# Performance work log

Measured on AMD Instinct MI355X. Metric: run time of the kernel, lower is better.

The kernel has to match this reference:

```python
import jax, jax.numpy as jnp
import numpy as np

M = 7
KSIZE = M + 1          # kernel height = 8
PAD = KSIZE // 2       # conv padding on seq dim = 4 -> output length L+1
NUM_KERNELS = 74


def setup_inputs() -> dict:
    key = jax.random.key(0)
    kx, kk = jax.random.split(key)
    x = jax.random.normal(kx, (256, 512, 7), dtype=jnp.float32)
    kernels = jax.random.normal(kk, (NUM_KERNELS, KSIZE, 3), dtype=jnp.float32)
    return {"x": x, "kernels": kernels}


def reference(x, kernels):
    # x: (B, L, C); kernels: (74, 8, 3)
    B, L, C = x.shape
    # Width-3 conv over width-1 input with padding 1: only the middle kernel
    # column (index 1) multiplies real data; the side columns hit zero padding.
    keff = kernels[:, :, 1]  # (74, 8)
    # Seq-dim cross-correlation with padding 4 and kernel 8 -> output length L+1.
    xp = jnp.pad(x, ((0, 0), (PAD, PAD), (0, 0)))  # (B, L+8, C)
    idx = jnp.arange(L + 1)[:, None] + jnp.arange(KSIZE)[None, :]  # (L+1, 8)
    win = xp[:, idx, :]  # (B, L+1, 8, C) sliding windows
    # First 73 kernels applied to every channel; outputs ordered channel-major
    # (channel outer, kernel inner) to match the torch append order.
    out_main = jnp.einsum('btjc,kj->btck', win, keff[:NUM_KERNELS - 1])
    out_main = out_main.reshape(B, L + 1, C * (NUM_KERNELS - 1))
    # Last kernel applied to one 'random' channel; fixed to channel 0 for
    # a deterministic reference (torch uses torch.randint at runtime).
    out_last = jnp.einsum('btj,j->bt', win[:, :, :, 0], keff[NUM_KERNELS - 1])
    out = jnp.concatenate([out_main, out_last[..., None]], axis=-1)  # (B, L+1, 73*C+1)
    # Faithful to torch: reshape (L+1)*(73*C+1) elems into (B, L, -1);
    # valid because 73*C+1 == 512 is divisible by L == 512.
    return out.reshape(B, L, -1)
```

## Files before the change

### kernel.cpp

```cpp
#include <hip/hip_runtime.h>


typedef float v2f __attribute__((ext_vector_type(2)));
typedef float v4f __attribute__((ext_vector_type(4)));

#define CDIM 7
#define TROWS 513
#define CHUNK 64
#define WIN_ROWS 72
#define WIN_ELEMS (WIN_ROWS * CDIM)

__device__ __forceinline__ int chan_of(int f) { return (f == 511) ? 0 : (f / 73); }
__device__ __forceinline__ int kidx_of(int f) { return (f == 511) ? 73 : (f % 73); }

__global__ __launch_bounds__(256, 8) void tok_conv_kernel(
    const float* __restrict__ x,
    const float* __restrict__ kern,
    float* __restrict__ out)
{
  __shared__ __align__(16) float lds[WIN_ELEMS];

  const int tid   = threadIdx.x;
  const int b     = blockIdx.y;
  const int chunk = blockIdx.x;
  const float* xb = x + b * (512 * CDIM);

  const int f0 = 2 * tid, f1 = f0 + 1;
  const int c0 = chan_of(f0), k0 = kidx_of(f0);
  const int c1 = chan_of(f1), k1 = kidx_of(f1);

  v2f kp[8];
#pragma unroll
  for (int j = 0; j < 8; ++j)
    kp[j] = (v2f){kern[k0 * 24 + j * 3 + 1], kern[k1 * 24 + j * 3 + 1]};

  if (chunk == 8) {
    v2f acc = {0.f, 0.f};
#pragma unroll
    for (int j = 0; j < 8; ++j) {
      const int p   = 508 + j;
      const bool ok = p < 512;
      const int bse = (ok ? p : 0) * CDIM;
      v2f w;
      w.x = ok ? xb[bse + c0] : 0.f;
      w.y = ok ? xb[bse + c1] : 0.f;
      acc += w * kp[j];
    }
    reinterpret_cast<v2f*>(out + ((size_t)b * TROWS + 512) * 512)[tid] = acc;
    return;
  }

  const int t0 = chunk * CHUNK;

  if (chunk >= 1 && chunk <= 6) {
    const v4f* src = reinterpret_cast<const v4f*>(xb + (t0 - 4) * CDIM);
    if (tid < WIN_ELEMS / 4)
      reinterpret_cast<v4f*>(lds)[tid] = src[tid];
  } else {
#pragma unroll
    for (int i = tid; i < WIN_ELEMS; i += 256) {
      const int r = i / CDIM;
      const int c = i - r * CDIM;
      const int p = t0 - 4 + r;
      lds[i] = ((unsigned)p < 512u) ? xb[p * CDIM + c] : 0.f;
    }
  }
  __syncthreads();

  int bx0 = c0, bx1 = c1;

  v2f w[8];
#pragma unroll
  for (int j = 0; j < 8; ++j)
    w[j] = (v2f){lds[bx0 + j * CDIM], lds[bx1 + j * CDIM]};

  v2f* orow = reinterpret_cast<v2f*>(out + ((size_t)b * TROWS + t0) * 512) + tid;

#pragma unroll 1
  for (int g = 0; g < 8; ++g) {
#pragma unroll
    for (int u = 0; u < 8; ++u) {
      v2f nv;
      nv.x = lds[bx0 + (u + 8) * CDIM];
      nv.y = lds[bx1 + (u + 8) * CDIM];

      v2f acc = {0.f, 0.f};
#pragma unroll
      for (int j = 0; j < 8; ++j)
        acc += w[(u + j) & 7] * kp[j];

      *orow = acc;
      orow += 256;

      w[u & 7] = nv;
    }
    bx0 += 8 * CDIM;
    bx1 += 8 * CDIM;
  }
}

extern "C" void kernel_launch(void* const* d_in, const int* in_sizes, int n_in,
                              void* d_out, int out_size, void* d_ws, size_t ws_size,
                              hipStream_t stream) {
  const float* x    = (const float*)d_in[0];
  const float* kern = (const float*)d_in[1];
  float* out        = (float*)d_out;

  dim3 grid(9, 256);
  tok_conv_kernel<<<grid, 256, 0, stream>>>(x, kern, out);
}
```

Baseline: 55.59 us.

## Use 16-byte output stores with paired-channel LDS layout and two-row interleave

Each thread now computes four adjacent output features per row and writes them as one 16-byte store, with the two halves of the block covering alternating rows. A second LDS staging pass rearranges the input window into channel pairs, so each sliding-window read is a single 8-byte load, including pairs that straddle two channels. The goal is fewer, wider global stores and fewer LDS reads per output. In exchange the kernel adds an extra LDS pass, an extra barrier and more registers, and the launch-bounds occupancy hint drops from 8 to 5.

```diff
diff --git a/kernel.cpp b/kernel.cpp
--- a/kernel.cpp
+++ b/kernel.cpp
@@ -8,33 +8,34 @@
 #define TROWS 513
 #define CHUNK 64
 #define WIN_ROWS 72
-#define WIN_ELEMS (WIN_ROWS * CDIM)
+#define RAW_ELEMS (WIN_ROWS * CDIM)
+#define NPAIRS 11
+#define PAIR_ITEMS (WIN_ROWS * NPAIRS)
 
 __device__ __forceinline__ int chan_of(int f) { return (f == 511) ? 0 : (f / 73); }
 __device__ __forceinline__ int kidx_of(int f) { return (f == 511) ? 73 : (f % 73); }
+__device__ __forceinline__ int pair_m(int f) {
+  const int cA = chan_of(f), cB = chan_of(f + 1);
+  return (cA == cB) ? cA : (cA == 6 ? 10 : 7 + (cA >> 1));
+}
 
-__global__ __launch_bounds__(256, 8) void tok_conv_kernel(
+__global__ __launch_bounds__(256, 5) void tok_conv_kernel(
     const float* __restrict__ x,
     const float* __restrict__ kern,
     float* __restrict__ out)
 {
-  __shared__ __align__(16) float lds[WIN_ELEMS];
+  __shared__ __align__(16) float raw[RAW_ELEMS];
+  __shared__ __align__(8)  v2f  pairs[PAIR_ITEMS];
 
   const int tid   = threadIdx.x;
   const int b     = blockIdx.y;
   const int chunk = blockIdx.x;
   const float* xb = x + b * (512 * CDIM);
 
-  const int f0 = 2 * tid, f1 = f0 + 1;
-  const int c0 = chan_of(f0), k0 = kidx_of(f0);
-  const int c1 = chan_of(f1), k1 = kidx_of(f1);
-
-  v2f kp[8];
-#pragma unroll
-  for (int j = 0; j < 8; ++j)
-    kp[j] = (v2f){kern[k0 * 24 + j * 3 + 1], kern[k1 * 24 + j * 3 + 1]};
-
   if (chunk == 8) {
+    const int f0 = 2 * tid, f1 = f0 + 1;
+    const int c0 = chan_of(f0), k0 = kidx_of(f0);
+    const int c1 = chan_of(f1), k1 = kidx_of(f1);
     v2f acc = {0.f, 0.f};
 #pragma unroll
     for (int j = 0; j < 8; ++j) {
@@ -44,58 +45,98 @@
       v2f w;
       w.x = ok ? xb[bse + c0] : 0.f;
       w.y = ok ? xb[bse + c1] : 0.f;
-      acc += w * kp[j];
+      const v2f kpj = {kern[k0 * 24 + j * 3 + 1], kern[k1 * 24 + j * 3 + 1]};
+      acc += w * kpj;
     }
     reinterpret_cast<v2f*>(out + ((size_t)b * TROWS + 512) * 512)[tid] = acc;
     return;
+  }
+
+  const int q    = tid & 127;
+  const int rpar = tid >> 7;
+  const int f0   = 4 * q;
+  const int m01  = pair_m(f0);
+  const int m23  = pair_m(f0 + 2);
+
+  v2f kp01[8], kp23[8];
+  {
+    const int k0 = kidx_of(f0),     k1 = kidx_of(f0 + 1);
+    const int k2 = kidx_of(f0 + 2), k3 = kidx_of(f0 + 3);
+#pragma unroll
+    for (int j = 0; j < 8; ++j) {
+      kp01[j] = (v2f){kern[k0 * 24 + j * 3 + 1], kern[k1 * 24 + j * 3 + 1]};
+      kp23[j] = (v2f){kern[k2 * 24 + j * 3 + 1], kern[k3 * 24 + j * 3 + 1]};
+    }
   }
 
   const int t0 = chunk * CHUNK;
 
   if (chunk >= 1 && chunk <= 6) {
     const v4f* src = reinterpret_cast<const v4f*>(xb + (t0 - 4) * CDIM);
-    if (tid < WIN_ELEMS / 4)
-      reinterpret_cast<v4f*>(lds)[tid] = src[tid];
+    if (tid < RAW_ELEMS / 4)
+      reinterpret_cast<v4f*>(raw)[tid] = src[tid];
   } else {
 #pragma unroll
-    for (int i = tid; i < WIN_ELEMS; i += 256) {
+    for (int i = tid; i < RAW_ELEMS; i += 256) {
       const int r = i / CDIM;
       const int c = i - r * CDIM;
       const int p = t0 - 4 + r;
-      lds[i] = ((unsigned)p < 512u) ? xb[p * CDIM + c] : 0.f;
+      raw[i] = ((unsigned)p < 512u) ? xb[p * CDIM + c] : 0.f;
     }
   }
   __syncthreads();
 
-  int bx0 = c0, bx1 = c1;
+#pragma unroll
+  for (int item = tid; item < PAIR_ITEMS; item += 256) {
+    const int r = item / NPAIRS;
+    const int m = item - r * NPAIRS;
+    const int cA = (m < 7) ? m : 2 * (m - 7);
+    const int cB = (m < 7) ? m : ((m == 10) ? 0 : cA + 1);
+    pairs[item] = (v2f){raw[r * CDIM + cA], raw[r * CDIM + cB]};
+  }
+  __syncthreads();
 
-  v2f w[8];
+  const v2f* pp01 = pairs + (rpar * NPAIRS + m01);
+  const v2f* pp23 = pairs + (rpar * NPAIRS + m23);
+
+  v2f wp01[8], wp23[8];
 #pragma unroll
-  for (int j = 0; j < 8; ++j)
-    w[j] = (v2f){lds[bx0 + j * CDIM], lds[bx1 + j * CDIM]};
+  for (int j = 0; j < 8; ++j) {
+    wp01[j] = pp01[j * NPAIRS];
+    wp23[j] = pp23[j * NPAIRS];
+  }
 
-  v2f* orow = reinterpret_cast<v2f*>(out + ((size_t)b * TROWS + t0) * 512) + tid;
+  v4f* orow =
+      reinterpret_cast<v4f*>(out + ((size_t)b * TROWS + t0 + rpar) * 512) + q;
 
 #pragma unroll 1
   for (int g = 0; g < 8; ++g) {
 #pragma unroll
-    for (int u = 0; u < 8; ++u) {
-      v2f nv;
-      nv.x = lds[bx0 + (u + 8) * CDIM];
-      nv.y = lds[bx1 + (u + 8) * CDIM];
+    for (int u = 0; u < 4; ++u) {
+      const int base = 2 * u;
 
-      v2f acc = {0.f, 0.f};
+      const v2f n01a = pp01[(base + 8) * NPAIRS];
+      const v2f n01b = pp01[(base + 9) * NPAIRS];
+      const v2f n23a = pp23[(base + 8) * NPAIRS];
+      const v2f n23b = pp23[(base + 9) * NPAIRS];
+
+      v2f a01 = {0.f, 0.f}, a23 = {0.f, 0.f};
 #pragma unroll
-      for (int j = 0; j < 8; ++j)
-        acc += w[(u + j) & 7] * kp[j];
+      for (int j = 0; j < 8; ++j) {
+        a01 += wp01[(base + j) & 7] * kp01[j];
+        a23 += wp23[(base + j) & 7] * kp23[j];
+      }
+      const v4f o = {a01.x, a01.y, a23.x, a23.y};
+      *orow = o;
+      orow += 2 * 128;
 
-      *orow = acc;
-      orow += 256;
-
-      w[u & 7] = nv;
+      wp01[base & 7]       = n01a;
+      wp01[(base + 1) & 7] = n01b;
+      wp23[base & 7]       = n23a;
+      wp23[(base + 1) & 7] = n23b;
     }
-    bx0 += 8 * CDIM;
-    bx1 += 8 * CDIM;
+    pp01 += 8 * NPAIRS;
+    pp23 += 8 * NPAIRS;
   }
 }
 
```

Measured after the change: 62.20 us. 11.9% more time.

## Stage output rows through double-buffered LDS for 16-byte global stores

Applied to the files above, without the earlier changes.

Each block now writes its computed outputs into two LDS buffers of four rows each instead of storing 8-byte values straight to global memory. It then copies each finished buffer to global memory with 16-byte vector stores, alternating buffers so the stores of one group overlap the computation of the next. The aim is wider, better-coalesced writes for this store-bound kernel. In exchange it adds 16 KB of LDS per block and two barriers per iteration, which may lower occupancy.

```diff
diff --git a/kernel.cpp b/kernel.cpp
--- a/kernel.cpp
+++ b/kernel.cpp
@@ -8,7 +8,7 @@
 #define TROWS 513
 #define CHUNK 64
 #define WIN_ROWS 72
-#define WIN_ELEMS (WIN_ROWS * CDIM)
+#define RAW_ELEMS (WIN_ROWS * CDIM)
 
 __device__ __forceinline__ int chan_of(int f) { return (f == 511) ? 0 : (f / 73); }
 __device__ __forceinline__ int kidx_of(int f) { return (f == 511) ? 73 : (f % 73); }
@@ -18,7 +18,9 @@
     const float* __restrict__ kern,
     float* __restrict__ out)
 {
-  __shared__ __align__(16) float lds[WIN_ELEMS];
+  __shared__ __align__(16) float raw[RAW_ELEMS];
+  __shared__ __align__(16) float buf0[4 * 512];
+  __shared__ __align__(16) float buf1[4 * 512];
 
   const int tid   = threadIdx.x;
   const int b     = blockIdx.y;
@@ -54,15 +56,15 @@
 
   if (chunk >= 1 && chunk <= 6) {
     const v4f* src = reinterpret_cast<const v4f*>(xb + (t0 - 4) * CDIM);
-    if (tid < WIN_ELEMS / 4)
-      reinterpret_cast<v4f*>(lds)[tid] = src[tid];
+    if (tid < RAW_ELEMS / 4)
+      reinterpret_cast<v4f*>(raw)[tid] = src[tid];
   } else {
 #pragma unroll
-    for (int i = tid; i < WIN_ELEMS; i += 256) {
+    for (int i = tid; i < RAW_ELEMS; i += 256) {
       const int r = i / CDIM;
       const int c = i - r * CDIM;
       const int p = t0 - 4 + r;
-      lds[i] = ((unsigned)p < 512u) ? xb[p * CDIM + c] : 0.f;
+      raw[i] = ((unsigned)p < 512u) ? xb[p * CDIM + c] : 0.f;
     }
   }
   __syncthreads();
@@ -72,31 +74,53 @@
   v2f w[8];
 #pragma unroll
   for (int j = 0; j < 8; ++j)
-    w[j] = (v2f){lds[bx0 + j * CDIM], lds[bx1 + j * CDIM]};
+    w[j] = (v2f){raw[bx0 + j * CDIM], raw[bx1 + j * CDIM]};
 
-  v2f* orow = reinterpret_cast<v2f*>(out + ((size_t)b * TROWS + t0) * 512) + tid;
+  v2f*       sb0 = reinterpret_cast<v2f*>(buf0) + tid;
+  v2f*       sb1 = reinterpret_cast<v2f*>(buf1) + tid;
+  const v4f* rb0 = reinterpret_cast<const v4f*>(buf0);
+  const v4f* rb1 = reinterpret_cast<const v4f*>(buf1);
+  v4f* dptr = reinterpret_cast<v4f*>(out + ((size_t)b * TROWS + t0) * 512);
 
 #pragma unroll 1
-  for (int g = 0; g < 8; ++g) {
+  for (int m = 0; m < 8; ++m) {
+    if (m) {
+      dptr[tid]       = rb1[tid];
+      dptr[tid + 256] = rb1[tid + 256];
+      dptr += 512;
+    }
 #pragma unroll
-    for (int u = 0; u < 8; ++u) {
-      v2f nv;
-      nv.x = lds[bx0 + (u + 8) * CDIM];
-      nv.y = lds[bx1 + (u + 8) * CDIM];
-
+    for (int u = 0; u < 4; ++u) {
+      v2f nv = {raw[bx0 + (u + 8) * CDIM], raw[bx1 + (u + 8) * CDIM]};
       v2f acc = {0.f, 0.f};
 #pragma unroll
       for (int j = 0; j < 8; ++j)
         acc += w[(u + j) & 7] * kp[j];
+      sb0[u * 256] = acc;
+      w[u] = nv;
+    }
+    __syncthreads();
 
-      *orow = acc;
-      orow += 256;
-
-      w[u & 7] = nv;
+    dptr[tid]       = rb0[tid];
+    dptr[tid + 256] = rb0[tid + 256];
+    dptr += 512;
+#pragma unroll
+    for (int u = 4; u < 8; ++u) {
+      v2f nv = {raw[bx0 + (u + 8) * CDIM], raw[bx1 + (u + 8) * CDIM]};
+      v2f acc = {0.f, 0.f};
+#pragma unroll
+      for (int j = 0; j < 8; ++j)
+        acc += w[(u + j) & 7] * kp[j];
+      sb1[(u - 4) * 256] = acc;
+      w[u] = nv;
     }
     bx0 += 8 * CDIM;
     bx1 += 8 * CDIM;
+    __syncthreads();
   }
+
+  dptr[tid]       = rb1[tid];
+  dptr[tid + 256] = rb1[tid + 256];
 }
 
 extern "C" void kernel_launch(void* const* d_in, const int* in_sizes, int n_in,
```

Measured after the change: 57.49 us. +3.4%, slower.
